# Optimization experiments

Hardware: AMD Instinct MI355X
Metric: run time of the kernel (lower is better)

The kernel has to match this reference:

```python
import jax, jax.numpy as jnp
import numpy as np

B, HQ, TQ, D = 8, 32, 128, 128      # batch, query heads, query len, head dim
HKV, MAXB, BS = 8, 64, 128          # kv heads, physical blocks, block size
NB = 32                              # logical blocks per sequence -> L = NB*BS = 4096
SCALE = D ** -0.5


def setup_inputs() -> dict:
    key = jax.random.key(0)
    k1, k2, k3, k4, k5 = jax.random.split(key, 5)
    q = jax.random.normal(k1, (B, HQ, TQ, D), dtype=jnp.float32)
    storage_k = jax.random.normal(k2, (B, HKV, MAXB, BS, D), dtype=jnp.float32)
    storage_v = jax.random.normal(k3, (B, HKV, MAXB, BS, D), dtype=jnp.float32)
    block_table = jax.random.randint(k4, (B, NB), 0, MAXB, dtype=jnp.int32)
    ctx_len = jax.random.randint(k5, (B,), 0, NB * BS, dtype=jnp.int32)
    return {"q": q, "storage_k": storage_k, "storage_v": storage_v,
            "block_table": block_table, "ctx_len": ctx_len}


def reference(q, storage_k, storage_v, block_table, ctx_len):
    """Paged KV-cache streaming-softmax decode attention with GQA repeat.

    q: [B,Hq,Tq,D]; storage_k/v: [B,Hkv,MAXB,BS,D]; block_table: [B,NB] int;
    ctx_len: [B] int (number of valid cached KV tokens per sequence).
    Equivalent to the torch block-wise online softmax: gather logical blocks,
    mask invalid/causal positions, one numerically-stable softmax.
    """
    Bq, Hq, Tq, Dh = q.shape
    Hkv = storage_k.shape[1]
    rep = Hq // Hkv
    bs = storage_k.shape[3]
    nb = block_table.shape[1]
    L = nb * bs

    # Gather logical KV blocks per batch: [B,Hkv,NB,BS,D] -> [B,Hkv,L,D]
    gather = jax.vmap(lambda s, bt: s[:, bt])
    k = gather(storage_k, block_table).reshape(Bq, Hkv, L, Dh)
    v = gather(storage_v, block_table).reshape(Bq, Hkv, L, Dh)

    # Validity (blen) + causal masks. q_abs = ctx_len + t, k_pos = bi*BS + off.
    k_pos = jnp.arange(L, dtype=jnp.int32)
    q_pos = ctx_len[:, None].astype(jnp.int32) + jnp.arange(Tq, dtype=jnp.int32)  # [B,Tq]
    mask = (k_pos[None, None, :] < ctx_len[:, None, None]) & \
           (k_pos[None, None, :] <= q_pos[:, :, None])                            # [B,Tq,L]

    # GQA: view Hq as (Hkv, rep) so each kv head serves its group without
    # materializing repeat_interleave'd K/V.
    qg = q.reshape(Bq, Hkv, rep, Tq, Dh)
    scores = jnp.einsum('bhrtd,bhld->bhrtl', qg, k) * SCALE                       # [B,Hkv,rep,Tq,L]
    scores = jnp.where(mask[:, None, None], scores, -jnp.inf)

    m = jnp.max(scores, axis=-1, keepdims=True)
    m = jnp.where(jnp.isfinite(m), m, 0.0)  # rows with no valid kv -> zeros out
    p = jnp.exp(scores - m)                  # masked entries: exp(-inf) = 0
    den = jnp.sum(p, axis=-1, keepdims=True)
    out = jnp.einsum('bhrtl,bhld->bhrtd', p, v) / jnp.maximum(den, 1e-9)
    return out.reshape(Bq, Hq, Tq, Dh)
```

## Files before the change

### kernel.cpp

```cpp
#include <hip/hip_runtime.h>
#include <hip/hip_bf16.h>
#include <math.h>

#define C_B    8
#define C_HQ   32
#define C_TQ   128
#define C_D    128
#define C_HKV  8
#define C_MAXB 64
#define C_BS   128
#define C_NB   32
#define SCALE_F 0.08838834764831845f

typedef __attribute__((ext_vector_type(8))) short bf16x8;
typedef __attribute__((ext_vector_type(4))) float f32x4;
typedef __attribute__((ext_vector_type(4))) short s16x4;

__device__ __forceinline__ unsigned f2bf(float f) {
    union { float f; unsigned u; } v; v.f = f;
    return (v.u + 0x7FFFu + ((v.u >> 16) & 1u)) >> 16;
}

__device__ __forceinline__ int swz(int row, int e) {
    return row * 256 + ((((e >> 3) ^ row) & 15) << 4) + ((e & 7) << 1);
}

__device__ __forceinline__ void quad_transpose(int cl, float& v0, float& v1, float& v2, float& v3) {
    float t0 = (cl & 1) ? v0 : v1;  float r0 = __shfl_xor(t0, 1, 64);
    float t1 = (cl & 1) ? v2 : v3;  float r1 = __shfl_xor(t1, 1, 64);
    float u0 = (cl & 1) ? r0 : v0;
    float u1 = (cl & 1) ? v1 : r0;
    float u2 = (cl & 1) ? r1 : v2;
    float u3 = (cl & 1) ? v3 : r1;
    float s0 = (cl & 2) ? u0 : u2;  float q0 = __shfl_xor(s0, 2, 64);
    float s1 = (cl & 2) ? u1 : u3;  float q1 = __shfl_xor(s1, 2, 64);
    v0 = (cl & 2) ? q0 : u0;
    v1 = (cl & 2) ? q1 : u1;
    v2 = (cl & 2) ? u2 : q0;
    v3 = (cl & 2) ? u3 : q1;
}

__global__ __launch_bounds__(256, 1)
void MultiAttention_6339371729052_kernel(const float* __restrict__ q,
                                         const float* __restrict__ sk,
                                         const float* __restrict__ sv,
                                         const int*   __restrict__ btab,
                                         const int*   __restrict__ ctxl,
                                         float*       __restrict__ out)
{
    __shared__ char lds[65536];
    char* ldsK = lds;
    char* ldsV = lds + 32768;

    const int bid = blockIdx.x;
    const int g  = ((bid >> 5) << 3) | (bid & 7);
    const int rp = (bid >> 3) & 3;
    const int b   = g >> 3;
    const int hkv = g & 7;
    const int hq  = hkv * 4 + rp;

    const int tid   = threadIdx.x;
    const int lane  = tid & 63;
    const int w     = tid >> 6;
    const int lq    = lane & 15;
    const int q4    = lane >> 4;
    const int lane3 = lane & 3;

    const int ctx  = ctxl[b];
    const int nblk = (ctx + C_BS - 1) / C_BS;

    bf16x8 qf[2][4];
    {
        const float* qb = q + ((size_t)(b * C_HQ + hq) * C_TQ) * C_D;
        #pragma unroll
        for (int mi = 0; mi < 2; mi++)
        #pragma unroll
        for (int kc = 0; kc < 4; kc++) {
            const float* p = qb + (w * 32 + mi * 16 + lq) * C_D + kc * 32 + q4 * 8;
            float4 x = *(const float4*)p;
            float4 y = *(const float4*)(p + 4);
            bf16x8 f;
            f[0] = (short)f2bf(x.x * SCALE_F); f[1] = (short)f2bf(x.y * SCALE_F);
            f[2] = (short)f2bf(x.z * SCALE_F); f[3] = (short)f2bf(x.w * SCALE_F);
            f[4] = (short)f2bf(y.x * SCALE_F); f[5] = (short)f2bf(y.y * SCALE_F);
            f[6] = (short)f2bf(y.z * SCALE_F); f[7] = (short)f2bf(y.w * SCALE_F);
            qf[mi][kc] = f;
        }
    }

    bf16x8 onesf;
    #pragma unroll
    for (int i = 0; i < 8; i++) onesf[i] = (short)0x3F80;

    f32x4 o[2][8];
    #pragma unroll
    for (int mi = 0; mi < 2; mi++)
        #pragma unroll
        for (int di = 0; di < 8; di++)
            o[mi][di] = (f32x4){0.f, 0.f, 0.f, 0.f};

    f32x4 lacc[2];
    lacc[0] = (f32x4){0.f, 0.f, 0.f, 0.f};
    lacc[1] = (f32x4){0.f, 0.f, 0.f, 0.f};

    float mrow[2][4];
    #pragma unroll
    for (int mi = 0; mi < 2; mi++)
        #pragma unroll
        for (int rr = 0; rr < 4; rr++) mrow[mi][rr] = -INFINITY;

    const size_t kvhead = (size_t)(b * C_HKV + hkv) * C_MAXB;

    for (int j = 0; j < nblk; j++) {
        const int pb = btab[b * C_NB + j];
        const float* kg = sk + (kvhead + pb) * (size_t)(C_BS * C_D);
        const float* vg = sv + (kvhead + pb) * (size_t)(C_BS * C_D);

        __syncthreads();

        #pragma unroll 4
        for (int it = 0; it < 16; it++) {
            int c  = tid + it * 256;
            int kv = c >> 5;
            int d0 = (c & 31) << 2;
            float4 x = *(const float4*)(kg + kv * C_D + d0);
            s16x4 pk;
            pk[0] = (short)f2bf(x.x); pk[1] = (short)f2bf(x.y);
            pk[2] = (short)f2bf(x.z); pk[3] = (short)f2bf(x.w);
            *(s16x4*)(ldsK + swz(kv, d0)) = pk;
        }
        #pragma unroll 4
        for (int it = 0; it < 16; it++) {
            int kvb = w * 32 + (it >> 1) * 4;
            int d0  = (it & 1) * 64 + ((lane >> 2) & 15) * 4;
            float4 x = *(const float4*)(vg + (kvb + lane3) * C_D + d0);
            float a = x.x, bb = x.y, cc = x.z, dd = x.w;
            quad_transpose(lane3, a, bb, cc, dd);
            s16x4 pk;
            pk[0] = (short)f2bf(a); pk[1] = (short)f2bf(bb);
            pk[2] = (short)f2bf(cc); pk[3] = (short)f2bf(dd);
            *(s16x4*)(ldsV + swz(d0 + lane3, kvb)) = pk;
        }

        __syncthreads();

        f32x4 s[2][8];
        #pragma unroll
        for (int mi = 0; mi < 2; mi++)
            #pragma unroll
            for (int nt = 0; nt < 8; nt++) s[mi][nt] = (f32x4){0.f, 0.f, 0.f, 0.f};
        #pragma unroll
        for (int kc = 0; kc < 4; kc++) {
            #pragma unroll
            for (int nt = 0; nt < 8; nt++) {
                bf16x8 kf = *(const bf16x8*)(ldsK + swz(nt * 16 + lq, kc * 32 + q4 * 8));
                s[0][nt] = __builtin_amdgcn_mfma_f32_16x16x32_bf16(qf[0][kc], kf, s[0][nt], 0, 0, 0);
                s[1][nt] = __builtin_amdgcn_mfma_f32_16x16x32_bf16(qf[1][kc], kf, s[1][nt], 0, 0, 0);
            }
        }

        if (j == nblk - 1) {
            int lim = ctx - j * C_BS;
            #pragma unroll
            for (int nt = 0; nt < 8; nt++) {
                bool bad = (nt * 16 + lq) >= lim;
                #pragma unroll
                for (int mi = 0; mi < 2; mi++)
                    #pragma unroll
                    for (int rr = 0; rr < 4; rr++)
                        s[mi][nt][rr] = bad ? -1e30f : s[mi][nt][rr];
            }
        }

        float al[2][4];
        #pragma unroll
        for (int mi = 0; mi < 2; mi++) {
            #pragma unroll
            for (int rr = 0; rr < 4; rr++) {
                float mx = fmaxf(fmaxf(fmaxf(s[mi][0][rr], s[mi][1][rr]), fmaxf(s[mi][2][rr], s[mi][3][rr])),
                                 fmaxf(fmaxf(s[mi][4][rr], s[mi][5][rr]), fmaxf(s[mi][6][rr], s[mi][7][rr])));
                mx = fmaxf(mx, __shfl_xor(mx, 1, 64));
                mx = fmaxf(mx, __shfl_xor(mx, 2, 64));
                mx = fmaxf(mx, __shfl_xor(mx, 4, 64));
                mx = fmaxf(mx, __shfl_xor(mx, 8, 64));
                float mn = fmaxf(mrow[mi][rr], mx);
                al[mi][rr] = __expf(mrow[mi][rr] - mn);
                mrow[mi][rr] = mn;
                #pragma unroll
                for (int nt = 0; nt < 8; nt++)
                    s[mi][nt][rr] = __expf(s[mi][nt][rr] - mn);
            }
            #pragma unroll
            for (int di = 0; di < 8; di++)
                #pragma unroll
                for (int rr = 0; rr < 4; rr++)
                    o[mi][di][rr] *= al[mi][rr];
            #pragma unroll
            for (int rr = 0; rr < 4; rr++)
                lacc[mi][rr] *= al[mi][rr];
        }

        __syncthreads();

        char* ldsP = ldsK + w * 8192;
        const int c4 = lq >> 2;
        #pragma unroll
        for (int mi = 0; mi < 2; mi++)
        #pragma unroll
        for (int nt = 0; nt < 8; nt++) {
            float a = s[mi][nt][0], bb = s[mi][nt][1], cc = s[mi][nt][2], dd = s[mi][nt][3];
            quad_transpose(lane3, a, bb, cc, dd);
            s16x4 pk;
            pk[0] = (short)f2bf(a); pk[1] = (short)f2bf(bb);
            pk[2] = (short)f2bf(cc); pk[3] = (short)f2bf(dd);
            *(s16x4*)(ldsP + swz(mi * 16 + q4 * 4 + lane3, nt * 16 + c4 * 4)) = pk;
        }

        #pragma unroll
        for (int kc2 = 0; kc2 < 4; kc2++) {
            bf16x8 ap0 = *(const bf16x8*)(ldsP + swz(lq,      kc2 * 32 + q4 * 8));
            bf16x8 ap1 = *(const bf16x8*)(ldsP + swz(16 + lq, kc2 * 32 + q4 * 8));
            lacc[0] = __builtin_amdgcn_mfma_f32_16x16x32_bf16(ap0, onesf, lacc[0], 0, 0, 0);
            lacc[1] = __builtin_amdgcn_mfma_f32_16x16x32_bf16(ap1, onesf, lacc[1], 0, 0, 0);
            #pragma unroll
            for (int di = 0; di < 8; di++) {
                bf16x8 bv = *(const bf16x8*)(ldsV + swz(di * 16 + lq, kc2 * 32 + q4 * 8));
                o[0][di] = __builtin_amdgcn_mfma_f32_16x16x32_bf16(ap0, bv, o[0][di], 0, 0, 0);
                o[1][di] = __builtin_amdgcn_mfma_f32_16x16x32_bf16(ap1, bv, o[1][di], 0, 0, 0);
            }
        }
    }

    float* ob = out + ((size_t)(b * C_HQ + hq) * C_TQ) * C_D;
    #pragma unroll
    for (int mi = 0; mi < 2; mi++)
    #pragma unroll
    for (int rr = 0; rr < 4; rr++) {
        float inv = 1.0f / fmaxf(lacc[mi][rr], 1e-9f);
        int t = w * 32 + mi * 16 + q4 * 4 + rr;
        #pragma unroll
        for (int di = 0; di < 8; di++)
            ob[(size_t)t * C_D + di * 16 + lq] = o[mi][di][rr] * inv;
    }
}

extern "C" void kernel_launch(void* const* d_in, const int* in_sizes, int n_in,
                              void* d_out, int out_size, void* d_ws, size_t ws_size,
                              hipStream_t stream) {
    const float* q  = (const float*)d_in[0];
    const float* sk = (const float*)d_in[1];
    const float* sv = (const float*)d_in[2];
    const int* btab = (const int*)d_in[3];
    const int* ctxl = (const int*)d_in[4];
    float* out = (float*)d_out;
    (void)in_sizes; (void)n_in; (void)out_size; (void)d_ws; (void)ws_size;

    hipLaunchKernelGGL(MultiAttention_6339371729052_kernel,
                       dim3(C_B * C_HKV * 4), dim3(256), 0, stream,
                       q, sk, sv, btab, ctxl, out);
}
```

Measured before the change: 715.6 us.

## Split KV blocks across workgroups with a separate softmax-combine kernel

Adds split-KV (flash-decoding style) parallelism: each (batch, q-head) tile is split into up to four workgroups over logical KV block ranges. Each split writes a normalized partial output in bf16 plus its row max and sum to workspace, and a second combine kernel merges them. The aim is to fill the GPU better than the original 256 workgroups and to balance uneven context lengths. The cost is extra workspace traffic, bf16 rounding of partials, a second launch, and the unnormalized sum reduction. It also raises launch bounds to two blocks per CU, which may limit registers.

```diff
diff --git a/kernel.cpp b/kernel.cpp
--- a/kernel.cpp
+++ b/kernel.cpp
@@ -40,23 +40,31 @@
     v3 = (cl & 2) ? u3 : q1;
 }
 
-__global__ __launch_bounds__(256, 1)
+__global__ __launch_bounds__(256, 2)
 void MultiAttention_6339371729052_kernel(const float* __restrict__ q,
                                          const float* __restrict__ sk,
                                          const float* __restrict__ sv,
                                          const int*   __restrict__ btab,
                                          const int*   __restrict__ ctxl,
-                                         float*       __restrict__ out)
+                                         float*       __restrict__ out,
+                                         unsigned short* __restrict__ Op,
+                                         float2*      __restrict__ st,
+                                         int S, int lgS)
 {
     __shared__ char lds[65536];
     char* ldsK = lds;
     char* ldsV = lds + 32768;
 
     const int bid = blockIdx.x;
-    const int g  = ((bid >> 5) << 3) | (bid & 7);
-    const int rp = (bid >> 3) & 3;
-    const int b   = g >> 3;
-    const int hkv = g & 7;
+    const int xcd = bid & 7;
+    const int r   = bid >> 3;
+    const int grp_in = r & (S * 8 - 1);
+    const int rp  = r >> (lgS + 3);
+    const int grp = xcd + 8 * grp_in;
+    const int bhkv  = grp >> lgS;
+    const int s_idx = grp & (S - 1);
+    const int b   = bhkv >> 3;
+    const int hkv = bhkv & 7;
     const int hq  = hkv * 4 + rp;
 
     const int tid   = threadIdx.x;
@@ -68,10 +76,21 @@
 
     const int ctx  = ctxl[b];
     const int nblk = (ctx + C_BS - 1) / C_BS;
+    const int bps  = C_NB >> lgS;
+    const int j0   = s_idx * bps;
+    const int j1   = min(nblk, j0 + bps);
+
+    const size_t rowbase = (size_t)(b * C_HQ + hq) * C_TQ;
+
+    if (S > 1 && j0 >= j1) {
+        if (tid < C_TQ)
+            st[(rowbase + tid) * S + s_idx] = make_float2(-1e30f, 0.0f);
+        return;
+    }
 
     bf16x8 qf[2][4];
     {
-        const float* qb = q + ((size_t)(b * C_HQ + hq) * C_TQ) * C_D;
+        const float* qb = q + rowbase * C_D;
         #pragma unroll
         for (int mi = 0; mi < 2; mi++)
         #pragma unroll
@@ -111,7 +130,7 @@
 
     const size_t kvhead = (size_t)(b * C_HKV + hkv) * C_MAXB;
 
-    for (int j = 0; j < nblk; j++) {
+    for (int j = j0; j < j1; j++) {
         const int pb = btab[b * C_NB + j];
         const float* kg = sk + (kvhead + pb) * (size_t)(C_BS * C_D);
         const float* vg = sv + (kvhead + pb) * (size_t)(C_BS * C_D);
@@ -231,17 +250,65 @@
         }
     }
 
-    float* ob = out + ((size_t)(b * C_HQ + hq) * C_TQ) * C_D;
-    #pragma unroll
-    for (int mi = 0; mi < 2; mi++)
-    #pragma unroll
-    for (int rr = 0; rr < 4; rr++) {
-        float inv = 1.0f / fmaxf(lacc[mi][rr], 1e-9f);
-        int t = w * 32 + mi * 16 + q4 * 4 + rr;
-        #pragma unroll
-        for (int di = 0; di < 8; di++)
-            ob[(size_t)t * C_D + di * 16 + lq] = o[mi][di][rr] * inv;
-    }
+    if (S == 1) {
+        float* ob = out + rowbase * C_D;
+        #pragma unroll
+        for (int mi = 0; mi < 2; mi++)
+        #pragma unroll
+        for (int rr = 0; rr < 4; rr++) {
+            float inv = 1.0f / fmaxf(lacc[mi][rr], 1e-9f);
+            int t = w * 32 + mi * 16 + q4 * 4 + rr;
+            #pragma unroll
+            for (int di = 0; di < 8; di++)
+                ob[(size_t)t * C_D + di * 16 + lq] = o[mi][di][rr] * inv;
+        }
+    } else {
+        #pragma unroll
+        for (int mi = 0; mi < 2; mi++)
+        #pragma unroll
+        for (int rr = 0; rr < 4; rr++) {
+            float l   = lacc[mi][rr];
+            float inv = (l > 0.f) ? 1.0f / l : 0.0f;
+            int t = w * 32 + mi * 16 + q4 * 4 + rr;
+            unsigned short* ob = Op + ((rowbase + t) * S + s_idx) * C_D;
+            #pragma unroll
+            for (int di = 0; di < 8; di++)
+                ob[di * 16 + lq] = (unsigned short)f2bf(o[mi][di][rr] * inv);
+            if (lq == 0)
+                st[(rowbase + t) * S + s_idx] = make_float2(mrow[mi][rr], l);
+        }
+    }
+}
+
+__global__ __launch_bounds__(256, 4)
+void combine_kernel(const unsigned short* __restrict__ Op,
+                    const float2* __restrict__ st,
+                    float* __restrict__ out, int S)
+{
+    const int wave = threadIdx.x >> 6;
+    const int lane = threadIdx.x & 63;
+    const size_t row = (size_t)blockIdx.x * 4 + wave;
+
+    const float2* sr = st + row * S;
+    float mstar = -INFINITY;
+    for (int s = 0; s < S; s++) {
+        float2 v = sr[s];
+        if (v.y > 0.f) mstar = fmaxf(mstar, v.x);
+    }
+    float acc0 = 0.f, acc1 = 0.f, wsum = 0.f;
+    for (int s = 0; s < S; s++) {
+        float2 v = sr[s];
+        float wgt = (v.y > 0.f) ? v.y * __expf(v.x - mstar) : 0.f;
+        wsum += wgt;
+        unsigned u = *(const unsigned*)(Op + (row * S + s) * C_D + lane * 2);
+        float o0 = __uint_as_float((u & 0xFFFFu) << 16);
+        float o1 = __uint_as_float((u >> 16) << 16);
+        acc0 += wgt * o0;
+        acc1 += wgt * o1;
+    }
+    float inv = (wsum > 0.f) ? 1.0f / wsum : 0.f;
+    out[row * C_D + lane * 2]     = acc0 * inv;
+    out[row * C_D + lane * 2 + 1] = acc1 * inv;
 }
 
 extern "C" void kernel_launch(void* const* d_in, const int* in_sizes, int n_in,
@@ -253,9 +320,25 @@
     const int* btab = (const int*)d_in[3];
     const int* ctxl = (const int*)d_in[4];
     float* out = (float*)d_out;
-    (void)in_sizes; (void)n_in; (void)out_size; (void)d_ws; (void)ws_size;
+    (void)in_sizes; (void)n_in; (void)out_size;
+
+    const size_t rows   = (size_t)C_B * C_HQ * C_TQ;
+    const size_t perSO  = rows * C_D * 2;
+    const size_t perSst = rows * sizeof(float2);
+
+    int S = 1, lgS = 0;
+    if (ws_size >= 4 * (perSO + perSst))      { S = 4; lgS = 2; }
+    else if (ws_size >= 2 * (perSO + perSst)) { S = 2; lgS = 1; }
+
+    unsigned short* Op = (unsigned short*)d_ws;
+    float2* st = (float2*)((char*)d_ws + (size_t)S * perSO);
 
     hipLaunchKernelGGL(MultiAttention_6339371729052_kernel,
-                       dim3(C_B * C_HKV * 4), dim3(256), 0, stream,
-                       q, sk, sv, btab, ctxl, out);
-}
+                       dim3(C_B * C_HKV * 4 * S), dim3(256), 0, stream,
+                       q, sk, sv, btab, ctxl, out, Op, st, S, lgS);
+    if (S > 1) {
+        hipLaunchKernelGGL(combine_kernel,
+                           dim3(rows / 4), dim3(256), 0, stream,
+                           Op, st, out, S);
+    }
+}
```

Result: faster. 627.1 us (-12.4%).
